# Performance work log

Measured on AMD Instinct MI355X. Metric: run time of the kernel, lower is better.

## Reference

```python
import jax, jax.numpy as jnp
import numpy as np

S, B, D, H = 1024, 16, 512, 8
DH = D // H  # 64


def setup_inputs() -> dict:
    key = jax.random.key(0)
    k1, k2, k3, k4, k5 = jax.random.split(key, 5)
    x = jax.random.normal(k1, (S, B, D), dtype=jnp.float32)
    # binary validity mask [B, S]: 1 = keep, 0 = masked out (matches torch usage)
    mask = (jax.random.uniform(k2, (B, S)) > 0.2).astype(jnp.float32)
    scale = 1.0 / np.sqrt(D)
    wq = jax.random.normal(k3, (H, DH, D), dtype=jnp.float32) * scale
    wk = jax.random.normal(k4, (H, DH, D), dtype=jnp.float32) * scale
    wv = jax.random.normal(k5, (H, DH, D), dtype=jnp.float32) * scale
    return {"x": x, "mask": mask, "wq": wq, "wk": wk, "wv": wv}


def reference(x, mask, wq, wk, wv):
    # x: [S, B, D]; mask: [B, S]; w*: [H, DH, D] (stacked bias-free Linear weights)
    dh = wq.shape[1]
    # per-hop projections for all hops at once (Linear: y = x @ W.T)
    q = jnp.einsum('sbd,hed->bhse', x, wq)  # [B,H,S,DH]
    k = jnp.einsum('sbd,hed->bhse', x, wk)
    v = jnp.einsum('sbd,hed->bhse', x, wv)
    scores = jnp.einsum('bhse,bhte->bhst', q, k)  # [B,H,S,S]
    inv_mask = (1.0 - mask)[:, None, None, :]      # broadcast over heads, query pos
    align = jnp.tanh(scores / jnp.sqrt(jnp.asarray(dh, x.dtype))) - 10000.0 * inv_mask
    align = jax.nn.softmax(align, axis=-1)
    out = jnp.einsum('bhst,bhte->bhse', align, v)  # [B,H,S,DH]
    s, b = x.shape[0], x.shape[1]
    # concat hops along feature dim, back to seq-first: [S, B, H*DH]
    return jnp.transpose(out, (2, 0, 1, 3)).reshape(s, b, -1)
```

## Files before the change

### kernel.cpp

```cpp
#include <hip/hip_runtime.h>
#include <stdint.h>
#include <stddef.h>

#define SS 1024
#define BB 16
#define DD 512
#define HH 8
#define DHH 64

typedef __attribute__((ext_vector_type(8))) short bf16x8;
typedef __attribute__((ext_vector_type(4))) float f32x4;
typedef __attribute__((ext_vector_type(16))) float f32x16;
typedef __attribute__((ext_vector_type(4))) float float4v;
typedef __attribute__((ext_vector_type(4))) unsigned short us4;

__device__ __forceinline__ unsigned short f2bf(float f) {
  union { float f; unsigned int u; } v; v.f = f;
  unsigned int x = v.u;
  return (unsigned short)((x + 0x7FFFu + ((x >> 16) & 1u)) >> 16);
}

#define GLDS16(dst, src)                                                                  \
  __builtin_amdgcn_global_load_lds(                                                      \
      (const __attribute__((address_space(1))) unsigned int*)(const void*)(src),         \
      (__attribute__((address_space(3))) unsigned int*)(void*)(dst), 16, 0, 0)

__global__ void cvt_kernel(const float* __restrict__ x,
                           const float* __restrict__ wq,
                           const float* __restrict__ wk,
                           const float* __restrict__ wv,
                           const float* __restrict__ mask,
                           unsigned short* __restrict__ xb,
                           unsigned short* __restrict__ wb,
                           float* __restrict__ maskq) {
  const int i = blockIdx.x * 256 + threadIdx.x;
  const int n_x4 = (SS * BB * DD) / 4;
  const int n_w4 = 3 * 65536;
  if (i < n_x4) {
    float4v v = ((const float4v*)x)[i];
    us4 o;
    o[0] = f2bf(v[0]); o[1] = f2bf(v[1]); o[2] = f2bf(v[2]); o[3] = f2bf(v[3]);
    ((us4*)xb)[i] = o;
  } else if (i < n_x4 + n_w4) {
    const int j = i - n_x4;
    const int sel = j >> 16;
    const int off4 = j & 65535;
    const float* wsrc = (sel == 0) ? wq : ((sel == 1) ? wk : wv);
    const float scale = (sel == 0) ? 0.36067376022224085f : 1.0f;
    float4v v = ((const float4v*)wsrc)[off4];
    us4 o;
    o[0] = f2bf(v[0] * scale); o[1] = f2bf(v[1] * scale);
    o[2] = f2bf(v[2] * scale); o[3] = f2bf(v[3] * scale);
    ((us4*)wb)[(sel << 16) + off4] = o;
  } else {
    const int j = i - n_x4 - n_w4;
    float4v mv = ((const float4v*)mask)[j];
    float4v o;
#pragma unroll
    for (int c = 0; c < 4; ++c) o[c] = (mv[c] > 0.5f) ? 0.f : -16384.f;
    ((float4v*)maskq)[j] = o;
  }
}

__global__ __launch_bounds__(256) void proj_kernel(
    const unsigned short* __restrict__ xb,
    const unsigned short* __restrict__ wb,
    unsigned short* __restrict__ qb,
    unsigned short* __restrict__ kb,
    unsigned short* __restrict__ vt) {
  const int bm = blockIdx.x * 128;
  const int bn = blockIdx.y * 128;
  const int b = blockIdx.z / 3;
  const int wsel = blockIdx.z % 3;

  __shared__ unsigned short At[128 * 32];
  __shared__ unsigned short Bt[128 * 32];
  __shared__ unsigned short OT[4][64 * 72];

  const int tid = threadIdx.x;
  const int w = tid >> 6;
  const int lane = tid & 63;

  const unsigned short* wptr = wb + wsel * (512 * DD);

  f32x4 acc[4][4];
#pragma unroll
  for (int mi = 0; mi < 4; ++mi)
#pragma unroll
    for (int ni = 0; ni < 4; ++ni) acc[mi][ni] = (f32x4){0.f, 0.f, 0.f, 0.f};

  const int m0 = (w & 1) * 64;
  const int n0 = (w >> 1) * 64;

  for (int kt = 0; kt < 16; ++kt) {
#pragma unroll
    for (int i = 0; i < 2; ++i) {
      const int idx8 = i * 256 + tid;
      const int r = idx8 >> 2;
      const int c8 = idx8 & 3;
      GLDS16(&At[(i * 256 + w * 64) * 8],
             xb + (size_t)(bm + r) * (BB * DD) + b * DD + kt * 32 + c8 * 8);
      GLDS16(&Bt[(i * 256 + w * 64) * 8],
             wptr + (size_t)(bn + r) * DD + kt * 32 + c8 * 8);
    }
    __syncthreads();
    bf16x8 af[4], bfr[4];
#pragma unroll
    for (int mi = 0; mi < 4; ++mi)
      af[mi] = *(const bf16x8*)&At[(m0 + mi * 16 + (lane & 15)) * 32 + (lane >> 4) * 8];
#pragma unroll
    for (int ni = 0; ni < 4; ++ni)
      bfr[ni] = *(const bf16x8*)&Bt[(n0 + ni * 16 + (lane & 15)) * 32 + (lane >> 4) * 8];
#pragma unroll
    for (int mi = 0; mi < 4; ++mi)
#pragma unroll
      for (int ni = 0; ni < 4; ++ni)
        acc[mi][ni] =
            __builtin_amdgcn_mfma_f32_16x16x32_bf16(af[mi], bfr[ni], acc[mi][ni], 0, 0, 0);
    __syncthreads();
  }

  const int h = (bn + n0) >> 6;
  unsigned short* OTw = &OT[w][0];
  if (wsel != 2) {
#pragma unroll
    for (int mi = 0; mi < 4; ++mi)
#pragma unroll
      for (int ni = 0; ni < 4; ++ni)
#pragma unroll
        for (int j = 0; j < 4; ++j)
          OTw[(mi * 16 + (lane >> 4) * 4 + j) * 72 + ni * 16 + (lane & 15)] =
              f2bf(acc[mi][ni][j]);
  } else {
#pragma unroll
    for (int mi = 0; mi < 4; ++mi)
#pragma unroll
      for (int ni = 0; ni < 4; ++ni) {
        us4 pk;
#pragma unroll
        for (int j = 0; j < 4; ++j) pk[j] = f2bf(acc[mi][ni][j]);
        *(us4*)&OTw[(ni * 16 + (lane & 15)) * 72 + mi * 16 + (lane >> 4) * 4] = pk;
      }
  }
  unsigned short* gout = (wsel == 0) ? qb : ((wsel == 1) ? kb : vt);
#pragma unroll
  for (int pass = 0; pass < 8; ++pass) {
    const int row = pass * 8 + (lane >> 3);
    bf16x8 vrow = *(const bf16x8*)&OTw[row * 72 + (lane & 7) * 8];
    size_t dst;
    if (wsel != 2)
      dst = ((size_t)(b * HH + h) * SS + (size_t)(bm + m0 + row)) * DHH + (lane & 7) * 8;
    else
      dst = ((size_t)(b * HH + h) * DHH + (size_t)row) * SS + (bm + m0) + (lane & 7) * 8;
    *(bf16x8*)&gout[dst] = vrow;
  }
}

__global__ __launch_bounds__(256, 4) void attn_kernel(
    const unsigned short* __restrict__ qb,
    const unsigned short* __restrict__ kb,
    const unsigned short* __restrict__ vt,
    const float* __restrict__ maskq,
    float* __restrict__ out) {
  const int id = blockIdx.x;
  const int xcd = id & 7;
  const int slot = id >> 3;
  const int bh = xcd * 16 + (slot >> 3);
  const int qt = slot & 7;
  const int b = bh >> 3;
  const int h = bh & 7;
  const int tid = threadIdx.x;
  const int w = tid >> 6;
  const int lane = tid & 63;
  const int l31 = lane & 31;
  const int hi32 = lane >> 5;
  const int sl = (l31 & 0x13) | ((l31 & 4) << 1) | ((l31 & 8) >> 1);

  __shared__ unsigned short Ks[2][64 * 64];
  __shared__ unsigned short Vs[2][64 * 64];
  __shared__ float rs_s[4][32];

  const size_t base_qk = (size_t)bh * SS * DHH;
  const int q0 = qt * 128 + w * 32;

  bf16x8 aq[4];
  {
    const unsigned short* qp = qb + base_qk + (size_t)(q0 + l31) * DHH + hi32 * 8;
    aq[0] = *(const bf16x8*)(qp);
    aq[1] = *(const bf16x8*)(qp + 16);
    aq[2] = *(const bf16x8*)(qp + 32);
    aq[3] = *(const bf16x8*)(qp + 48);
  }

  const int sr0 = w * 16 + (lane >> 3);
  const int sxb = (((lane & 7) ^ (lane >> 3)) << 4);
  const unsigned short* ksrc0 = kb + base_qk + (size_t)sr0 * DHH + (sxb >> 1);
  const unsigned short* ksrc1 = ksrc0 + 8 * DHH;
  const unsigned short* vsrc0 =
      vt + (size_t)bh * DHH * SS + (size_t)sr0 * SS + (sxb >> 1);
  const unsigned short* vsrc1 = vsrc0 + 8 * SS;

#define STAGE(bb, kt2)                                                       \
  do {                                                                       \
    GLDS16(&Ks[bb][(w * 16) * 64], ksrc0 + (size_t)(kt2) * (64 * DHH));      \
    GLDS16(&Ks[bb][(w * 16 + 8) * 64], ksrc1 + (size_t)(kt2) * (64 * DHH));  \
    GLDS16(&Vs[bb][(w * 16) * 64], vsrc0 + (size_t)(kt2) * 64);              \
    GLDS16(&Vs[bb][(w * 16 + 8) * 64], vsrc1 + (size_t)(kt2) * 64);          \
  } while (0)

  STAGE(0, 0);

  f32x16 accO[2];
#pragma unroll
  for (int n = 0; n < 2; ++n)
#pragma unroll
    for (int i = 0; i < 16; ++i) accO[n][i] = 0.f;
  float rs = 0.f;
  const float* mrow = maskq + b * SS;

  __syncthreads();

  int buf = 0;
  for (int kt = 0; kt < 16; ++kt) {
    if (kt < 15) STAGE(buf ^ 1, kt + 1);
    const char* Kb = (const char*)&Ks[buf][0];
    const char* Vb = (const char*)&Vs[buf][0];

#pragma unroll
    for (int T = 0; T < 2; ++T) {
      const int krow = T * 32 + sl;
      const int ksw = (krow & 7) << 4;
      f32x16 sc = {};
      __builtin_amdgcn_s_setprio(1);
#pragma unroll
      for (int ks = 0; ks < 4; ++ks) {
        bf16x8 kf = *(const bf16x8*)(Kb + krow * 128 + ((ks * 32 + hi32 * 16) ^ ksw));
        sc = __builtin_amdgcn_mfma_f32_32x32x16_bf16(kf, aq[ks], sc, 0, 0, 0);
      }
      __builtin_amdgcn_s_setprio(0);
      unsigned int pu[16];
#pragma unroll
      for (int g = 0; g < 4; ++g) {
        float4v mv = *(const float4v*)&mrow[kt * 64 + T * 32 + (g >> 1) * 16 +
                                            hi32 * 8 + (g & 1) * 4];
        float a0 = 1.f + __builtin_amdgcn_exp2f(sc[g * 4 + 0]);
        float a1 = 1.f + __builtin_amdgcn_exp2f(sc[g * 4 + 1]);
        float a2 = 1.f + __builtin_amdgcn_exp2f(sc[g * 4 + 2]);
        float a3 = 1.f + __builtin_amdgcn_exp2f(sc[g * 4 + 3]);
        float p01 = a0 * a1, p23 = a2 * a3;
        float rq = __builtin_amdgcn_rcpf(p01 * p23);
        float r01 = p23 * rq, r23 = p01 * rq;
        float r[4];
        r[0] = a1 * r01; r[1] = a0 * r01; r[2] = a3 * r23; r[3] = a2 * r23;
#pragma unroll
        for (int i = 0; i < 4; ++i) {
          float p = __builtin_amdgcn_exp2f(__builtin_fmaf(r[i], -2.88539008178f, mv[i]));
          rs += p;
          union { float f; unsigned int u; } cv;
          cv.f = p;
          pu[g * 4 + i] = cv.u;
        }
      }
      union { unsigned int u[4]; bf16x8 v; } f0, f1;
#pragma unroll
      for (int m = 0; m < 4; ++m) {
        f0.u[m] = __builtin_amdgcn_perm(pu[2 * m + 1], pu[2 * m], 0x07060302u);
        f1.u[m] = __builtin_amdgcn_perm(pu[8 + 2 * m + 1], pu[8 + 2 * m], 0x07060302u);
      }
      __builtin_amdgcn_s_setprio(1);
#pragma unroll
      for (int n = 0; n < 2; ++n) {
        const int vrow = n * 32 + l31;
        const int vsw = (vrow & 7) << 4;
        bf16x8 bv0 = *(const bf16x8*)(Vb + vrow * 128 + (((T * 2 + 0) * 32 + hi32 * 16) ^ vsw));
        bf16x8 bv1 = *(const bf16x8*)(Vb + vrow * 128 + (((T * 2 + 1) * 32 + hi32 * 16) ^ vsw));
        accO[n] = __builtin_amdgcn_mfma_f32_32x32x16_bf16(f0.v, bv0, accO[n], 0, 0, 0);
        accO[n] = __builtin_amdgcn_mfma_f32_32x32x16_bf16(f1.v, bv1, accO[n], 0, 0, 0);
      }
      __builtin_amdgcn_s_setprio(0);
    }
    __syncthreads();
    buf ^= 1;
  }
#undef STAGE

  rs += __shfl_xor(rs, 32, 64);
  if (hi32 == 0) rs_s[w][l31] = __builtin_amdgcn_rcpf(rs);
  float4v ri[4];
#pragma unroll
  for (int g = 0; g < 4; ++g) ri[g] = *(const float4v*)&rs_s[w][g * 8 + hi32 * 4];

#pragma unroll
  for (int n = 0; n < 2; ++n)
#pragma unroll
    for (int g = 0; g < 4; ++g)
#pragma unroll
      for (int i = 0; i < 4; ++i) {
        const int qrow = q0 + g * 8 + hi32 * 4 + i;
        out[((size_t)qrow * BB + b) * DD + h * DHH + n * 32 + l31] =
            accO[n][g * 4 + i] * ri[g][i];
      }
}

extern "C" void kernel_launch(void* const* d_in, const int* in_sizes, int n_in,
                              void* d_out, int out_size, void* d_ws, size_t ws_size,
                              hipStream_t stream) {
  const float* x = (const float*)d_in[0];
  const float* mask = (const float*)d_in[1];
  const float* wq = (const float*)d_in[2];
  const float* wk = (const float*)d_in[3];
  const float* wv = (const float*)d_in[4];
  float* out = (float*)d_out;

  char* ws = (char*)d_ws;
  unsigned short* xb = (unsigned short*)(ws);
  unsigned short* wb = (unsigned short*)(ws + (16ull << 20));
  float* maskq = (float*)(ws + (17ull << 20) + (512ull << 10));
  unsigned short* qb = (unsigned short*)(ws + (18ull << 20));
  unsigned short* kb = (unsigned short*)(ws + (34ull << 20));
  unsigned short* vt = (unsigned short*)(ws + (50ull << 20));

  cvt_kernel<<<dim3(8976), 256, 0, stream>>>(x, wq, wk, wv, mask, xb, wb, maskq);
  proj_kernel<<<dim3(8, 4, 48), 256, 0, stream>>>(xb, wb, qb, kb, vt);
  attn_kernel<<<dim3(1024), 256, 0, stream>>>(qb, kb, vt, maskq, out);
}
```

Baseline: 116.4 us.

## Replace tanh-softmax exp chain with rational approximation and register-staged K/V loads

The tanh-then-exp softmax numerator is replaced by a rational function of exp2(score), (19u²+22u+7)/(7u²+22u+19), clamped, which removes the second exp per element. The binary mask is multiplied in directly instead of being added as a precomputed additive bias, so the mask-conversion part of the convert kernel is dropped. K/V staging moves from global_load_lds to register loads issued early and written to the swizzled LDS buffer after compute. The rational form is an approximation of exp(-2·tanh) that may be inexact, and the multiplicative mask relies on the mask values being exactly 0 or 1.

```diff
diff --git a/kernel.cpp b/kernel.cpp
--- a/kernel.cpp
+++ b/kernel.cpp
@@ -13,6 +13,7 @@
 typedef __attribute__((ext_vector_type(16))) float f32x16;
 typedef __attribute__((ext_vector_type(4))) float float4v;
 typedef __attribute__((ext_vector_type(4))) unsigned short us4;
+typedef __attribute__((ext_vector_type(4))) unsigned int uint4v;
 
 __device__ __forceinline__ unsigned short f2bf(float f) {
   union { float f; unsigned int u; } v; v.f = f;
@@ -29,19 +30,16 @@
                            const float* __restrict__ wq,
                            const float* __restrict__ wk,
                            const float* __restrict__ wv,
-                           const float* __restrict__ mask,
                            unsigned short* __restrict__ xb,
-                           unsigned short* __restrict__ wb,
-                           float* __restrict__ maskq) {
+                           unsigned short* __restrict__ wb) {
   const int i = blockIdx.x * 256 + threadIdx.x;
   const int n_x4 = (SS * BB * DD) / 4;
-  const int n_w4 = 3 * 65536;
   if (i < n_x4) {
     float4v v = ((const float4v*)x)[i];
     us4 o;
     o[0] = f2bf(v[0]); o[1] = f2bf(v[1]); o[2] = f2bf(v[2]); o[3] = f2bf(v[3]);
     ((us4*)xb)[i] = o;
-  } else if (i < n_x4 + n_w4) {
+  } else {
     const int j = i - n_x4;
     const int sel = j >> 16;
     const int off4 = j & 65535;
@@ -52,13 +50,6 @@
     o[0] = f2bf(v[0] * scale); o[1] = f2bf(v[1] * scale);
     o[2] = f2bf(v[2] * scale); o[3] = f2bf(v[3] * scale);
     ((us4*)wb)[(sel << 16) + off4] = o;
-  } else {
-    const int j = i - n_x4 - n_w4;
-    float4v mv = ((const float4v*)mask)[j];
-    float4v o;
-#pragma unroll
-    for (int c = 0; c < 4; ++c) o[c] = (mv[c] > 0.5f) ? 0.f : -16384.f;
-    ((float4v*)maskq)[j] = o;
   }
 }
 
@@ -160,7 +151,7 @@
     const unsigned short* __restrict__ qb,
     const unsigned short* __restrict__ kb,
     const unsigned short* __restrict__ vt,
-    const float* __restrict__ maskq,
+    const float* __restrict__ mask,
     float* __restrict__ out) {
   const int id = blockIdx.x;
   const int xcd = id & 7;
@@ -192,23 +183,11 @@
     aq[3] = *(const bf16x8*)(qp + 48);
   }
 
-  const int sr0 = w * 16 + (lane >> 3);
-  const int sxb = (((lane & 7) ^ (lane >> 3)) << 4);
-  const unsigned short* ksrc0 = kb + base_qk + (size_t)sr0 * DHH + (sxb >> 1);
-  const unsigned short* ksrc1 = ksrc0 + 8 * DHH;
-  const unsigned short* vsrc0 =
-      vt + (size_t)bh * DHH * SS + (size_t)sr0 * SS + (sxb >> 1);
-  const unsigned short* vsrc1 = vsrc0 + 8 * SS;
-
-#define STAGE(bb, kt2)                                                       \
-  do {                                                                       \
-    GLDS16(&Ks[bb][(w * 16) * 64], ksrc0 + (size_t)(kt2) * (64 * DHH));      \
-    GLDS16(&Ks[bb][(w * 16 + 8) * 64], ksrc1 + (size_t)(kt2) * (64 * DHH));  \
-    GLDS16(&Vs[bb][(w * 16) * 64], vsrc0 + (size_t)(kt2) * 64);              \
-    GLDS16(&Vs[bb][(w * 16 + 8) * 64], vsrc1 + (size_t)(kt2) * 64);          \
-  } while (0)
-
-  STAGE(0, 0);
+  const int srow = w * 16 + (lane >> 3);
+  const unsigned short* kg = kb + base_qk + (size_t)srow * DHH + (lane & 7) * 8;
+  const unsigned short* vg =
+      vt + (size_t)bh * DHH * SS + (size_t)srow * SS + (lane & 7) * 8;
+  const int lofs = srow * 128 + (((lane & 7) ^ (lane >> 3)) << 4);
 
   f32x16 accO[2];
 #pragma unroll
@@ -216,13 +195,31 @@
 #pragma unroll
     for (int i = 0; i < 16; ++i) accO[n][i] = 0.f;
   float rs = 0.f;
-  const float* mrow = maskq + b * SS;
-
+  const float* mrow = mask + b * SS;
+
+  {
+    uint4v a0 = *(const uint4v*)kg;
+    uint4v a1 = *(const uint4v*)(kg + 8 * DHH);
+    uint4v a2 = *(const uint4v*)vg;
+    uint4v a3 = *(const uint4v*)(vg + 8 * SS);
+    *(uint4v*)((char*)&Ks[0][0] + lofs) = a0;
+    *(uint4v*)((char*)&Ks[0][0] + lofs + 1024) = a1;
+    *(uint4v*)((char*)&Vs[0][0] + lofs) = a2;
+    *(uint4v*)((char*)&Vs[0][0] + lofs + 1024) = a3;
+  }
   __syncthreads();
 
   int buf = 0;
   for (int kt = 0; kt < 16; ++kt) {
-    if (kt < 15) STAGE(buf ^ 1, kt + 1);
+    uint4v nk0, nk1, nv0, nv1;
+    if (kt < 15) {
+      const unsigned short* kgn = kg + (size_t)(kt + 1) * (64 * DHH);
+      const unsigned short* vgn = vg + (size_t)(kt + 1) * 64;
+      nk0 = *(const uint4v*)kgn;
+      nk1 = *(const uint4v*)(kgn + 8 * DHH);
+      nv0 = *(const uint4v*)vgn;
+      nv1 = *(const uint4v*)(vgn + 8 * SS);
+    }
     const char* Kb = (const char*)&Ks[buf][0];
     const char* Vb = (const char*)&Vs[buf][0];
 
@@ -243,23 +240,31 @@
       for (int g = 0; g < 4; ++g) {
         float4v mv = *(const float4v*)&mrow[kt * 64 + T * 32 + (g >> 1) * 16 +
                                             hi32 * 8 + (g & 1) * 4];
-        float a0 = 1.f + __builtin_amdgcn_exp2f(sc[g * 4 + 0]);
-        float a1 = 1.f + __builtin_amdgcn_exp2f(sc[g * 4 + 1]);
-        float a2 = 1.f + __builtin_amdgcn_exp2f(sc[g * 4 + 2]);
-        float a3 = 1.f + __builtin_amdgcn_exp2f(sc[g * 4 + 3]);
-        float p01 = a0 * a1, p23 = a2 * a3;
+        float u0 = __builtin_fminf(__builtin_amdgcn_exp2f(sc[g * 4 + 0]), 16384.f);
+        float u1 = __builtin_fminf(__builtin_amdgcn_exp2f(sc[g * 4 + 1]), 16384.f);
+        float u2 = __builtin_fminf(__builtin_amdgcn_exp2f(sc[g * 4 + 2]), 16384.f);
+        float u3 = __builtin_fminf(__builtin_amdgcn_exp2f(sc[g * 4 + 3]), 16384.f);
+        float n0 = __builtin_fmaf(__builtin_fmaf(19.f, u0, 22.f), u0, 7.f);
+        float n1 = __builtin_fmaf(__builtin_fmaf(19.f, u1, 22.f), u1, 7.f);
+        float n2 = __builtin_fmaf(__builtin_fmaf(19.f, u2, 22.f), u2, 7.f);
+        float n3 = __builtin_fmaf(__builtin_fmaf(19.f, u3, 22.f), u3, 7.f);
+        float d0 = __builtin_fmaf(__builtin_fmaf(7.f, u0, 22.f), u0, 19.f);
+        float d1 = __builtin_fmaf(__builtin_fmaf(7.f, u1, 22.f), u1, 19.f);
+        float d2 = __builtin_fmaf(__builtin_fmaf(7.f, u2, 22.f), u2, 19.f);
+        float d3 = __builtin_fmaf(__builtin_fmaf(7.f, u3, 22.f), u3, 19.f);
+        float p01 = d0 * d1, p23 = d2 * d3;
         float rq = __builtin_amdgcn_rcpf(p01 * p23);
         float r01 = p23 * rq, r23 = p01 * rq;
-        float r[4];
-        r[0] = a1 * r01; r[1] = a0 * r01; r[2] = a3 * r23; r[3] = a2 * r23;
-#pragma unroll
-        for (int i = 0; i < 4; ++i) {
-          float p = __builtin_amdgcn_exp2f(__builtin_fmaf(r[i], -2.88539008178f, mv[i]));
-          rs += p;
-          union { float f; unsigned int u; } cv;
-          cv.f = p;
-          pu[g * 4 + i] = cv.u;
-        }
+        float qr0 = d1 * r01, qr1 = d0 * r01, qr2 = d3 * r23, qr3 = d2 * r23;
+        float p0 = (mv[0] * n0) * qr0;
+        float p1 = (mv[1] * n1) * qr1;
+        float p2 = (mv[2] * n2) * qr2;
+        float p3 = (mv[3] * n3) * qr3;
+        rs += p0; rs += p1; rs += p2; rs += p3;
+        union { float f; unsigned int u; } c0, c1, c2, c3;
+        c0.f = p0; c1.f = p1; c2.f = p2; c3.f = p3;
+        pu[g * 4 + 0] = c0.u; pu[g * 4 + 1] = c1.u;
+        pu[g * 4 + 2] = c2.u; pu[g * 4 + 3] = c3.u;
       }
       union { unsigned int u[4]; bf16x8 v; } f0, f1;
 #pragma unroll
@@ -279,10 +284,18 @@
       }
       __builtin_amdgcn_s_setprio(0);
     }
+
+    if (kt < 15) {
+      char* Kn = (char*)&Ks[buf ^ 1][0];
+      char* Vn = (char*)&Vs[buf ^ 1][0];
+      *(uint4v*)(Kn + lofs) = nk0;
+      *(uint4v*)(Kn + lofs + 1024) = nk1;
+      *(uint4v*)(Vn + lofs) = nv0;
+      *(uint4v*)(Vn + lofs + 1024) = nv1;
+    }
     __syncthreads();
     buf ^= 1;
   }
-#undef STAGE
 
   rs += __shfl_xor(rs, 32, 64);
   if (hi32 == 0) rs_s[w][l31] = __builtin_amdgcn_rcpf(rs);
@@ -315,12 +328,11 @@
   char* ws = (char*)d_ws;
   unsigned short* xb = (unsigned short*)(ws);
   unsigned short* wb = (unsigned short*)(ws + (16ull << 20));
-  float* maskq = (float*)(ws + (17ull << 20) + (512ull << 10));
   unsigned short* qb = (unsigned short*)(ws + (18ull << 20));
   unsigned short* kb = (unsigned short*)(ws + (34ull << 20));
   unsigned short* vt = (unsigned short*)(ws + (50ull << 20));
 
-  cvt_kernel<<<dim3(8976), 256, 0, stream>>>(x, wq, wk, wv, mask, xb, wb, maskq);
+  cvt_kernel<<<dim3(8960), 256, 0, stream>>>(x, wq, wk, wv, xb, wb);
   proj_kernel<<<dim3(8, 4, 48), 256, 0, stream>>>(xb, wb, qb, kb, vt);
-  attn_kernel<<<dim3(1024), 256, 0, stream>>>(qb, kb, vt, maskq, out);
-}
+  attn_kernel<<<dim3(1024), 256, 0, stream>>>(qb, kb, vt, mask, out);
+}
```

New measurement: 133.4 us. 1.15x slower.
